# Kernel optimization log

Hardware: AMD Instinct MI355X
Metric: run time of the kernel (lower is better)

Reference implementation:

```python
import jax, jax.numpy as jnp
import numpy as np

L, H, D, V, TMAX = 12, 12, 768, 50257, 1024
B, T = 2, 1024
HD = D // H
EPS = 1e-5


def new_gelu(x):
    return 0.5 * x * (1.0 + jnp.tanh(jnp.sqrt(2.0 / jnp.pi) * (x + 0.044715 * x ** 3)))


def layer_norm(x, w, b):
    mu = jnp.mean(x, axis=-1, keepdims=True)
    var = jnp.var(x, axis=-1, keepdims=True)
    return (x - mu) * jax.lax.rsqrt(var + EPS) * w + b


def setup_inputs() -> dict:
    key = jax.random.key(0)
    ks = jax.random.split(key, 12)
    s = 0.02
    return {
        "idx": jax.random.randint(ks[0], (B, T), 0, V),
        "wte": jax.random.normal(ks[1], (V, D), jnp.float32) * s,
        "wpe": jax.random.normal(ks[2], (TMAX, D), jnp.float32) * s,
        "ln1_w": jnp.ones((L, D), jnp.float32),
        "ln1_b": jnp.zeros((L, D), jnp.float32),
        "attn_w": jax.random.normal(ks[3], (L, D, 3 * D), jnp.float32) * s,
        "attn_b": jnp.zeros((L, 3 * D), jnp.float32),
        "proj_w": jax.random.normal(ks[4], (L, D, D), jnp.float32) * (s / jnp.sqrt(2.0 * L)),
        "proj_b": jnp.zeros((L, D), jnp.float32),
        "ln2_w": jnp.ones((L, D), jnp.float32),
        "ln2_b": jnp.zeros((L, D), jnp.float32),
        "fc_w": jax.random.normal(ks[5], (L, D, 4 * D), jnp.float32) * s,
        "fc_b": jnp.zeros((L, 4 * D), jnp.float32),
        "fc2_w": jax.random.normal(ks[6], (L, 4 * D, D), jnp.float32) * (s / jnp.sqrt(2.0 * L)),
        "fc2_b": jnp.zeros((L, D), jnp.float32),
        "lnf_w": jnp.ones((D,), jnp.float32),
        "lnf_b": jnp.zeros((D,), jnp.float32),
        "lm_head_w": jax.random.normal(ks[7], (D, V), jnp.float32) * s,
    }


def _gpt_forward(idx, wte, wpe, ln1_w, ln1_b, attn_w, attn_b, proj_w, proj_b,
                 ln2_w, ln2_b, fc_w, fc_b, fc2_w, fc2_b, lnf_w, lnf_b, lm_head_w):
    b, t = idx.shape
    x = wte[idx] + wpe[:t][None, :, :]  # [B,T,D]
    causal = jnp.tril(jnp.ones((t, t), bool))  # [T,T]
    scale = 1.0 / jnp.sqrt(jnp.asarray(HD, x.dtype))

    layer_params = {
        "ln1_w": ln1_w, "ln1_b": ln1_b, "attn_w": attn_w, "attn_b": attn_b,
        "proj_w": proj_w, "proj_b": proj_b, "ln2_w": ln2_w, "ln2_b": ln2_b,
        "fc_w": fc_w, "fc_b": fc_b, "fc2_w": fc2_w, "fc2_b": fc2_b,
    }

    def block(x, p):
        h = layer_norm(x, p["ln1_w"], p["ln1_b"])
        qkv = h @ p["attn_w"] + p["attn_b"]  # [B,T,3D]
        q, k, v = jnp.split(qkv, 3, axis=-1)
        q = q.reshape(b, t, H, HD)
        k = k.reshape(b, t, H, HD)
        v = v.reshape(b, t, H, HD)
        att = jnp.einsum("bqhd,bkhd->bhqk", q, k) * scale
        att = jnp.where(causal[None, None, :, :], att, -jnp.inf)
        att = jax.nn.softmax(att, axis=-1)
        y = jnp.einsum("bhqk,bkhd->bqhd", att, v).reshape(b, t, D)
        x = x + y @ p["proj_w"] + p["proj_b"]
        h2 = layer_norm(x, p["ln2_w"], p["ln2_b"])
        m = new_gelu(h2 @ p["fc_w"] + p["fc_b"])
        x = x + m @ p["fc2_w"] + p["fc2_b"]
        return x, None

    x, _ = jax.lax.scan(block, x, layer_params)
    x = layer_norm(x, lnf_w, lnf_b)
    logits = x @ lm_head_w  # [B,T,V]
    return logits


def reference(idx, wte, wpe, ln1_w, ln1_b, attn_w, attn_b, proj_w, proj_b,
              ln2_w, ln2_b, fc_w, fc_b, fc2_w, fc2_b, lnf_w, lnf_b, lm_head_w):
    return _gpt_forward(idx, wte, wpe, ln1_w, ln1_b, attn_w, attn_b, proj_w, proj_b,
                        ln2_w, ln2_b, fc_w, fc_b, fc2_w, fc2_b, lnf_w, lnf_b, lm_head_w)
```

## Files before the change

kernel.cpp:

```cpp
#include <hip/hip_runtime.h>
#include <math.h>

#define Bsz  2
#define Tlen 1024
#define Dm   768
#define Hh   12
#define HDm  64
#define Ll   12
#define Vv   50257
#define Mrows (Bsz * Tlen)

typedef __attribute__((ext_vector_type(8))) short short8;
typedef __attribute__((ext_vector_type(4))) float f32x4;

__device__ __forceinline__ float bf2f(unsigned short u) {
  union { unsigned int i; float f; } v; v.i = ((unsigned int)u) << 16; return v.f;
}
__device__ __forceinline__ unsigned short f2bf(float f) {
  union { float f; unsigned int i; } v; v.f = f;
  unsigned int u = v.i;
  return (unsigned short)((u + 0x7FFFu + ((u >> 16) & 1u)) >> 16);
}
__device__ __forceinline__ float gelu_f(float x) {
  const float c = 0.7978845608028654f;
  return 0.5f * x * (1.0f + tanhf(c * (x + 0.044715f * x * x * x)));
}

__device__ __forceinline__ void gl_lds16(const unsigned short* g, unsigned short* l) {
  __builtin_amdgcn_global_load_lds(
      (const __attribute__((address_space(1))) unsigned int*)g,
      (__attribute__((address_space(3))) unsigned int*)l, 16, 0, 0);
}


__global__ void embed_kernel(const int* __restrict__ idx, const float* __restrict__ wte,
                             const float* __restrict__ wpe, float* __restrict__ x) {
  int i = (blockIdx.x * 256 + threadIdx.x) * 4;
  int d = i % Dm;
  int bt = i / Dm;
  int t = bt % Tlen;
  int tok = idx[bt];
  float4 a = *(const float4*)(wte + (size_t)tok * Dm + d);
  float4 p = *(const float4*)(wpe + (size_t)t * Dm + d);
  float4 r; r.x = a.x + p.x; r.y = a.y + p.y; r.z = a.z + p.z; r.w = a.w + p.w;
  *(float4*)(x + i) = r;
}

__global__ __launch_bounds__(256) void ln_wave(const float* __restrict__ x,
                                               const float* __restrict__ w,
                                               const float* __restrict__ b,
                                               unsigned short* __restrict__ out) {
  int tid = threadIdx.x, wv = tid >> 6, l = tid & 63;
  int row = blockIdx.x * 4 + wv;
  const float* xr = x + (size_t)row * Dm;
  float4 v[3];
  float s = 0.f, s2 = 0.f;
#pragma unroll
  for (int i = 0; i < 3; ++i) {
    v[i] = *(const float4*)(xr + l * 4 + i * 256);
    s += v[i].x + v[i].y + v[i].z + v[i].w;
    s2 += v[i].x * v[i].x + v[i].y * v[i].y + v[i].z * v[i].z + v[i].w * v[i].w;
  }
#pragma unroll
  for (int o = 1; o < 64; o <<= 1) {
    s += __shfl_xor(s, o, 64);
    s2 += __shfl_xor(s2, o, 64);
  }
  float mu = s * (1.0f / Dm);
  float var = s2 * (1.0f / Dm) - mu * mu;
  float rstd = rsqrtf(var + 1e-5f);
  unsigned short* yr = out + (size_t)row * Dm;
#pragma unroll
  for (int i = 0; i < 3; ++i) {
    float4 wv4 = *(const float4*)(w + l * 4 + i * 256);
    float4 bv4 = *(const float4*)(b + l * 4 + i * 256);
    ushort4 o4;
    o4.x = f2bf((v[i].x - mu) * rstd * wv4.x + bv4.x);
    o4.y = f2bf((v[i].y - mu) * rstd * wv4.y + bv4.y);
    o4.z = f2bf((v[i].z - mu) * rstd * wv4.z + bv4.z);
    o4.w = f2bf((v[i].w - mu) * rstd * wv4.w + bv4.w);
    *(ushort4*)(yr + l * 4 + i * 256) = o4;
  }
}

__global__ __launch_bounds__(256) void tconv_kernel(const float* __restrict__ W, int ldw,
                                                    int nValid, unsigned short* __restrict__ WT,
                                                    int K) {
  __shared__ float S[32][33];
  int n0 = blockIdx.x * 32, k0 = blockIdx.y * 32;
  int t = threadIdx.x;
  int nc = t & 31, kr0 = t >> 5;
#pragma unroll
  for (int i = 0; i < 4; ++i) {
    int kr = kr0 + i * 8;
    S[kr][nc] = (n0 + nc < nValid) ? W[(size_t)(k0 + kr) * ldw + n0 + nc] : 0.f;
  }
  __syncthreads();
  int r = t >> 3, c4 = (t & 7) * 4;
  ushort4 o;
  o.x = f2bf(S[c4 + 0][r]); o.y = f2bf(S[c4 + 1][r]);
  o.z = f2bf(S[c4 + 2][r]); o.w = f2bf(S[c4 + 3][r]);
  *(ushort4*)(WT + (size_t)(n0 + r) * K + k0 + c4) = o;
}

__global__ __launch_bounds__(256) void tconv4_kernel(
    const float* __restrict__ wA, const float* __restrict__ wP,
    const float* __restrict__ wF, const float* __restrict__ wF2,
    unsigned short* __restrict__ oA, unsigned short* __restrict__ oP,
    unsigned short* __restrict__ oF, unsigned short* __restrict__ oF2) {
  int bid = blockIdx.x;
  const float* W; unsigned short* WT; int ldw, K, ntn, local;
  if (bid < 1728)      { W = wA;  WT = oA;  ldw = 2304; K = 768;  ntn = 72; local = bid; }
  else if (bid < 2304) { W = wP;  WT = oP;  ldw = 768;  K = 768;  ntn = 24; local = bid - 1728; }
  else if (bid < 4608) { W = wF;  WT = oF;  ldw = 3072; K = 768;  ntn = 96; local = bid - 2304; }
  else                 { W = wF2; WT = oF2; ldw = 768;  K = 3072; ntn = 24; local = bid - 4608; }
  int n0 = (local % ntn) * 32, k0 = (local / ntn) * 32;
  __shared__ float S[32][33];
  int t = threadIdx.x;
  int nc = t & 31, kr0 = t >> 5;
#pragma unroll
  for (int i = 0; i < 4; ++i) {
    int kr = kr0 + i * 8;
    S[kr][nc] = W[(size_t)(k0 + kr) * ldw + n0 + nc];
  }
  __syncthreads();
  int r = t >> 3, c4 = (t & 7) * 4;
  ushort4 o;
  o.x = f2bf(S[c4 + 0][r]); o.y = f2bf(S[c4 + 1][r]);
  o.z = f2bf(S[c4 + 2][r]); o.w = f2bf(S[c4 + 3][r]);
  *(ushort4*)(WT + (size_t)(n0 + r) * K + k0 + c4) = o;
}

template<bool XMAP>
__global__ __launch_bounds__(256) void gemm_big(
    const unsigned short* __restrict__ A, const unsigned short* __restrict__ B, int K,
    const float* __restrict__ bias, const float* __restrict__ res,
    float* __restrict__ outF, unsigned short* __restrict__ outB,
    int ldc, int nValid, int act, int nColTiles) {
  int brow, bcol;
  if (XMAP) {
    int b = blockIdx.x, xcd = b & 7, slot = b >> 3;
    bcol = xcd + 8 * (slot >> 4);
    brow = slot & 15;
    if (bcol >= nColTiles) return;
  } else {
    bcol = blockIdx.x; brow = blockIdx.y;
  }
  __shared__ alignas(16) unsigned short As[2][128][32];
  __shared__ alignas(16) unsigned short Bs[2][128][32];
  int tid = threadIdx.x;
  int rowBase = brow * 128, colBase = bcol * 128;
  int w = tid >> 6, l = tid & 63;
  int wr = w >> 1, wc = w & 1;
  int srow = tid >> 2;
  int skk = (((tid & 3) ^ ((tid >> 3) & 3))) * 8;
  const unsigned short* aSrc = A + (size_t)(rowBase + srow) * K + skk;
  const unsigned short* bSrc = B + (size_t)(colBase + srow) * K + skk;

  f32x4 acc[4][4];
#pragma unroll
  for (int m = 0; m < 4; ++m)
#pragma unroll
    for (int n = 0; n < 4; ++n) acc[m][n] = (f32x4){0.f, 0.f, 0.f, 0.f};

  int fr = l & 15, fq = l >> 4;
  int kslot = (fq ^ ((fr >> 1) & 3)) * 8;

  gl_lds16(aSrc, &As[0][w * 16][0]);
  gl_lds16(aSrc + (size_t)64 * K, &As[0][w * 16 + 64][0]);
  gl_lds16(bSrc, &Bs[0][w * 16][0]);
  gl_lds16(bSrc + (size_t)64 * K, &Bs[0][w * 16 + 64][0]);

  int nIt = K >> 5;
  for (int it = 0; it < nIt; ++it) {
    int cur = it & 1;
    int k0 = it * 32;
    if (it + 1 < nIt) {
      int nx = cur ^ 1;
      gl_lds16(aSrc + k0 + 32, &As[nx][w * 16][0]);
      gl_lds16(aSrc + (size_t)64 * K + k0 + 32, &As[nx][w * 16 + 64][0]);
      gl_lds16(bSrc + k0 + 32, &Bs[nx][w * 16][0]);
      gl_lds16(bSrc + (size_t)64 * K + k0 + 32, &Bs[nx][w * 16 + 64][0]);
      asm volatile("s_waitcnt vmcnt(4)" ::: "memory");
    } else {
      asm volatile("s_waitcnt vmcnt(0)" ::: "memory");
    }
    asm volatile("s_barrier" ::: "memory");

    short8 af[4], bfr[4];
#pragma unroll
    for (int m = 0; m < 4; ++m)
      af[m] = *(const short8*)&As[cur][wr * 64 + m * 16 + fr][kslot];
#pragma unroll
    for (int n = 0; n < 4; ++n)
      bfr[n] = *(const short8*)&Bs[cur][wc * 64 + n * 16 + fr][kslot];
#pragma unroll
    for (int m = 0; m < 4; ++m)
#pragma unroll
      for (int n = 0; n < 4; ++n)
        acc[m][n] = __builtin_amdgcn_mfma_f32_16x16x32_bf16(af[m], bfr[n], acc[m][n], 0, 0, 0);
    asm volatile("s_barrier" ::: "memory");
  }

#pragma unroll
  for (int m = 0; m < 4; ++m) {
    int row = rowBase + wr * 64 + m * 16 + fq * 4;
#pragma unroll
    for (int n = 0; n < 4; ++n) {
      int col = colBase + wc * 64 + n * 16 + fr;
      if (col >= nValid) continue;
      float bv = bias ? bias[col] : 0.f;
#pragma unroll
      for (int j = 0; j < 4; ++j) {
        float v = acc[m][n][j] + bv;
        if (act) v = gelu_f(v);
        if (res) v += res[(size_t)(row + j) * ldc + col];
        if (outF) outF[(size_t)(row + j) * ldc + col] = v;
        else      outB[(size_t)(row + j) * ldc + col] = f2bf(v);
      }
    }
  }
}

__global__ __launch_bounds__(256) void gemm_bf16_sm(
    const unsigned short* __restrict__ A, const unsigned short* __restrict__ B, int K,
    const float* __restrict__ bias,
    float* __restrict__ outF, unsigned short* __restrict__ outB,
    int ldc, int act) {
  __shared__ alignas(16) unsigned short As[2][64][32];
  __shared__ alignas(16) unsigned short Bs[2][128][32];
  int tid = threadIdx.x;
  int rowBase = blockIdx.y * 64;
  int colBase = blockIdx.x * 128;
  int w = tid >> 6, l = tid & 63;
  int fr = l & 15, fq = l >> 4;

  int srow = l >> 2;
  int skk = (((l & 3) ^ ((l >> 3) & 3))) * 8;
  const unsigned short* aSrc = A + (size_t)(rowBase + w * 16 + srow) * K + skk;
  const unsigned short* bSrc = B + (size_t)(colBase + w * 16 + srow) * K + skk;
  int kslot = (fq ^ ((fr >> 1) & 3)) * 8;

  f32x4 acc[4][2];
#pragma unroll
  for (int m = 0; m < 4; ++m)
#pragma unroll
    for (int n = 0; n < 2; ++n) acc[m][n] = (f32x4){0.f, 0.f, 0.f, 0.f};

  gl_lds16(aSrc, &As[0][w * 16][0]);
  gl_lds16(bSrc, &Bs[0][w * 16][0]);
  gl_lds16(bSrc + (size_t)64 * K, &Bs[0][w * 16 + 64][0]);

  int nIt = K >> 5;
  for (int it = 0; it < nIt; ++it) {
    int cur = it & 1;
    int k0 = it * 32;
    if (it + 1 < nIt) {
      int nx = cur ^ 1;
      gl_lds16(aSrc + k0 + 32, &As[nx][w * 16][0]);
      gl_lds16(bSrc + k0 + 32, &Bs[nx][w * 16][0]);
      gl_lds16(bSrc + (size_t)64 * K + k0 + 32, &Bs[nx][w * 16 + 64][0]);
      asm volatile("s_waitcnt vmcnt(3)" ::: "memory");
    } else {
      asm volatile("s_waitcnt vmcnt(0)" ::: "memory");
    }
    asm volatile("s_barrier" ::: "memory");

    short8 af[4], bfr[2];
#pragma unroll
    for (int m = 0; m < 4; ++m)
      af[m] = *(const short8*)&As[cur][m * 16 + fr][kslot];
#pragma unroll
    for (int n = 0; n < 2; ++n)
      bfr[n] = *(const short8*)&Bs[cur][w * 32 + n * 16 + fr][kslot];
#pragma unroll
    for (int m = 0; m < 4; ++m)
#pragma unroll
      for (int n = 0; n < 2; ++n)
        acc[m][n] = __builtin_amdgcn_mfma_f32_16x16x32_bf16(af[m], bfr[n], acc[m][n], 0, 0, 0);
    asm volatile("s_barrier" ::: "memory");
  }

#pragma unroll
  for (int m = 0; m < 4; ++m) {
    int row = rowBase + m * 16 + fq * 4;
#pragma unroll
    for (int n = 0; n < 2; ++n) {
      int col = colBase + w * 32 + n * 16 + fr;
      float bv = bias ? bias[col] : 0.f;
#pragma unroll
      for (int j = 0; j < 4; ++j) {
        float v = acc[m][n][j] + bv;
        if (act) v = gelu_f(v);
        if (outF) outF[(size_t)(row + j) * ldc + col] = v;
        else      outB[(size_t)(row + j) * ldc + col] = f2bf(v);
      }
    }
  }
}

__global__ __launch_bounds__(256) void gemm_splitk(
    const unsigned short* __restrict__ A, const unsigned short* __restrict__ B, int K,
    int Klen, const float* __restrict__ bias, float* __restrict__ outF, int ldc) {
  __shared__ alignas(16) unsigned short As[2][64][32];
  __shared__ alignas(16) unsigned short Bs[2][128][32];
  int tid = threadIdx.x;
  int rowBase = blockIdx.y * 64;
  int colBase = blockIdx.x * 128;
  int Koff = blockIdx.z * Klen;
  int w = tid >> 6, l = tid & 63;
  int fr = l & 15, fq = l >> 4;

  int srow = l >> 2;
  int skk = (((l & 3) ^ ((l >> 3) & 3))) * 8;
  const unsigned short* aSrc = A + (size_t)(rowBase + w * 16 + srow) * K + Koff + skk;
  const unsigned short* bSrc = B + (size_t)(colBase + w * 16 + srow) * K + Koff + skk;
  int kslot = (fq ^ ((fr >> 1) & 3)) * 8;

  f32x4 acc[4][2];
#pragma unroll
  for (int m = 0; m < 4; ++m)
#pragma unroll
    for (int n = 0; n < 2; ++n) acc[m][n] = (f32x4){0.f, 0.f, 0.f, 0.f};

  gl_lds16(aSrc, &As[0][w * 16][0]);
  gl_lds16(bSrc, &Bs[0][w * 16][0]);
  gl_lds16(bSrc + (size_t)64 * K, &Bs[0][w * 16 + 64][0]);

  int nIt = Klen >> 5;
  for (int it = 0; it < nIt; ++it) {
    int cur = it & 1;
    int k0 = it * 32;
    if (it + 1 < nIt) {
      int nx = cur ^ 1;
      gl_lds16(aSrc + k0 + 32, &As[nx][w * 16][0]);
      gl_lds16(bSrc + k0 + 32, &Bs[nx][w * 16][0]);
      gl_lds16(bSrc + (size_t)64 * K + k0 + 32, &Bs[nx][w * 16 + 64][0]);
      asm volatile("s_waitcnt vmcnt(3)" ::: "memory");
    } else {
      asm volatile("s_waitcnt vmcnt(0)" ::: "memory");
    }
    asm volatile("s_barrier" ::: "memory");

    short8 af[4], bfr[2];
#pragma unroll
    for (int m = 0; m < 4; ++m)
      af[m] = *(const short8*)&As[cur][m * 16 + fr][kslot];
#pragma unroll
    for (int n = 0; n < 2; ++n)
      bfr[n] = *(const short8*)&Bs[cur][w * 32 + n * 16 + fr][kslot];
#pragma unroll
    for (int m = 0; m < 4; ++m)
#pragma unroll
      for (int n = 0; n < 2; ++n)
        acc[m][n] = __builtin_amdgcn_mfma_f32_16x16x32_bf16(af[m], bfr[n], acc[m][n], 0, 0, 0);
    asm volatile("s_barrier" ::: "memory");
  }

  bool addBias = (blockIdx.z == 0);
#pragma unroll
  for (int m = 0; m < 4; ++m) {
    int row = rowBase + m * 16 + fq * 4;
#pragma unroll
    for (int n = 0; n < 2; ++n) {
      int col = colBase + w * 32 + n * 16 + fr;
      float bv = addBias ? bias[col] : 0.f;
#pragma unroll
      for (int j = 0; j < 4; ++j) {
        unsafeAtomicAdd(&outF[(size_t)(row + j) * ldc + col], acc[m][n][j] + bv);
      }
    }
  }
}

__global__ __launch_bounds__(256) void attn_mfma(const unsigned short* __restrict__ qkv,
                                                 unsigned short* __restrict__ y) {
  int bx = blockIdx.x;
  int qt = 15 - (bx / 24);
  int bh = bx % 24;
  int h  = bh % Hh;
  int b  = bh / Hh;
  int q0 = qt * 64;
  int tid = threadIdx.x;
  int w = tid >> 6, l = tid & 63;
  int g = l >> 4, fr = l & 15;

  __shared__ alignas(16) unsigned short Kl[2][4096];
  __shared__ alignas(16) unsigned short Vt[4096];
  __shared__ alignas(16) unsigned short Pl[4][1024];

  const size_t rs = 3 * Dm;
  const unsigned short* base = qkv + (size_t)(b * Tlen) * rs + h * HDm;

  short8 qf[2];
  {
    const unsigned short* qrow = base + (size_t)(q0 + w * 16 + fr) * rs;
    qf[0] = *(const short8*)(qrow + g * 8);
    qf[1] = *(const short8*)(qrow + g * 8 + 32);
  }

  int vt_t = tid >> 2, vt_dc = tid & 3;
  uint4 v0r, v1r;

  f32x4 oAcc[4];
#pragma unroll
  for (int nd = 0; nd < 4; ++nd) oAcc[nd] = (f32x4){0.f, 0.f, 0.f, 0.f};
  float mRun[4] = {-1e30f, -1e30f, -1e30f, -1e30f};
  float lRun[4] = {0.f, 0.f, 0.f, 0.f};

  unsigned short* Pw = &Pl[w][0];
  int nkt = qt + 1;

  {
#pragma unroll
    for (int i = 0; i < 2; ++i) {
      int c = i * 256 + tid;
      int t = c >> 3, cl = c & 7;
      int dch = cl ^ (t & 7);
      gl_lds16(base + (size_t)t * rs + Dm + dch * 8, &Kl[0][(i * 256 + w * 64) * 8]);
    }
    const unsigned short* p = base + (size_t)vt_t * rs + 2 * Dm + vt_dc * 16;
    v0r = *(const uint4*)p;
    v1r = *(const uint4*)(p + 8);
  }

  for (int kt = 0; kt < nkt; ++kt) {
    int cur = kt & 1;
    int kbase = kt * 64;
    asm volatile("s_waitcnt vmcnt(0)" ::: "memory");
    __builtin_amdgcn_s_barrier();

    {
      union { uint4 u; unsigned short s[8]; } a, bb;
      a.u = v0r; bb.u = v1r;
#pragma unroll
      for (int j = 0; j < 8; ++j) {
        int d = vt_dc * 16 + j;
        Vt[d * 64 + (vt_t ^ ((d & 7) << 3))] = a.s[j];
        int d2 = d + 8;
        Vt[d2 * 64 + (vt_t ^ ((d2 & 7) << 3))] = bb.s[j];
      }
    }
    if (kt + 1 < nkt) {
      int kb = kbase + 64;
#pragma unroll
      for (int i = 0; i < 2; ++i) {
        int c = i * 256 + tid;
        int t = c >> 3, cl = c & 7;
        int dch = cl ^ (t & 7);
        gl_lds16(base + (size_t)(kb + t) * rs + Dm + dch * 8,
                 &Kl[cur ^ 1][(i * 256 + w * 64) * 8]);
      }
      const unsigned short* p = base + (size_t)(kb + vt_t) * rs + 2 * Dm + vt_dc * 16;
      v0r = *(const uint4*)p;
      v1r = *(const uint4*)(p + 8);
    }
    asm volatile("s_waitcnt lgkmcnt(0)" ::: "memory");
    __builtin_amdgcn_s_barrier();

    f32x4 sAcc[4];
#pragma unroll
    for (int nt = 0; nt < 4; ++nt) sAcc[nt] = (f32x4){0.f, 0.f, 0.f, 0.f};
#pragma unroll
    for (int ks = 0; ks < 2; ++ks)
#pragma unroll
      for (int nt = 0; nt < 4; ++nt) {
        int kcol = nt * 16 + fr;
        short8 kf = *(const short8*)&Kl[cur][kcol * 64 + ((g * 8 + ks * 32) ^ ((kcol & 7) << 3))];
        sAcc[nt] = __builtin_amdgcn_mfma_f32_16x16x32_bf16(qf[ks], kf, sAcc[nt], 0, 0, 0);
      }

    float corr[4];
#pragma unroll
    for (int j = 0; j < 4; ++j) {
      int qg = q0 + w * 16 + g * 4 + j;
      float tm = -1e30f;
#pragma unroll
      for (int nt = 0; nt < 4; ++nt) {
        float s = sAcc[nt][j] * 0.125f;
        int tg = kbase + nt * 16 + fr;
        if (tg > qg) s = -1e30f;
        sAcc[nt][j] = s;
        tm = fmaxf(tm, s);
      }
      tm = fmaxf(tm, __shfl_xor(tm, 1, 16));
      tm = fmaxf(tm, __shfl_xor(tm, 2, 16));
      tm = fmaxf(tm, __shfl_xor(tm, 4, 16));
      tm = fmaxf(tm, __shfl_xor(tm, 8, 16));
      float mN = fmaxf(mRun[j], tm);
      corr[j] = __expf(mRun[j] - mN);
      mRun[j] = mN;
      float ps = 0.f;
#pragma unroll
      for (int nt = 0; nt < 4; ++nt) {
        float p = __expf(sAcc[nt][j] - mN);
        sAcc[nt][j] = p;
        ps += p;
      }
      ps += __shfl_xor(ps, 1, 16);
      ps += __shfl_xor(ps, 2, 16);
      ps += __shfl_xor(ps, 4, 16);
      ps += __shfl_xor(ps, 8, 16);
      lRun[j] = lRun[j] * corr[j] + ps;
    }

#pragma unroll
    for (int nt = 0; nt < 4; ++nt)
#pragma unroll
      for (int j = 0; j < 4; ++j) {
        int q = g * 4 + j;
        int t = nt * 16 + fr;
        Pw[q * 64 + (t ^ ((q & 7) << 3))] = f2bf(sAcc[nt][j]);
      }
#pragma unroll
    for (int nd = 0; nd < 4; ++nd)
#pragma unroll
      for (int j = 0; j < 4; ++j) oAcc[nd][j] *= corr[j];

#pragma unroll
    for (int ks = 0; ks < 2; ++ks) {
      short8 pf = *(const short8*)&Pw[fr * 64 + ((g * 8 + ks * 32) ^ ((fr & 7) << 3))];
#pragma unroll
      for (int nd = 0; nd < 4; ++nd) {
        int d = nd * 16 + fr;
        short8 vf = *(const short8*)&Vt[d * 64 + ((g * 8 + ks * 32) ^ ((fr & 7) << 3))];
        oAcc[nd] = __builtin_amdgcn_mfma_f32_16x16x32_bf16(pf, vf, oAcc[nd], 0, 0, 0);
      }
    }
  }

#pragma unroll
  for (int j = 0; j < 4; ++j) {
    float inv = 1.0f / lRun[j];
    int q = q0 + w * 16 + g * 4 + j;
    unsigned short* yr = y + (size_t)(b * Tlen + q) * Dm + h * HDm + fr;
#pragma unroll
    for (int nd = 0; nd < 4; ++nd)
      yr[nd * 16] = f2bf(oAcc[nd][j] * inv);
  }
}

extern "C" void kernel_launch(void* const* d_in, const int* in_sizes, int n_in,
                              void* d_out, int out_size, void* d_ws, size_t ws_size,
                              hipStream_t stream) {
  const int*   idx    = (const int*)d_in[0];
  const float* wte    = (const float*)d_in[1];
  const float* wpe    = (const float*)d_in[2];
  const float* ln1_w  = (const float*)d_in[3];
  const float* ln1_b  = (const float*)d_in[4];
  const float* attn_w = (const float*)d_in[5];
  const float* attn_b = (const float*)d_in[6];
  const float* proj_w = (const float*)d_in[7];
  const float* proj_b = (const float*)d_in[8];
  const float* ln2_w  = (const float*)d_in[9];
  const float* ln2_b  = (const float*)d_in[10];
  const float* fc_w   = (const float*)d_in[11];
  const float* fc_b   = (const float*)d_in[12];
  const float* fc2_w  = (const float*)d_in[13];
  const float* fc2_b  = (const float*)d_in[14];
  const float* lnf_w  = (const float*)d_in[15];
  const float* lnf_b  = (const float*)d_in[16];
  const float* lmw    = (const float*)d_in[17];
  float* out = (float*)d_out;

  float* x = (float*)d_ws;
  unsigned short* qkvb = (unsigned short*)(x + (size_t)Mrows * Dm);
  unsigned short* xb   = qkvb + (size_t)Mrows * 3 * Dm;
  unsigned short* yb   = xb + (size_t)Mrows * Dm;
  unsigned short* mb   = yb + (size_t)Mrows * Dm;
  unsigned short* wbuf = mb + (size_t)Mrows * 4 * Dm;
  unsigned short* wAttn = wbuf;
  unsigned short* wProj = wAttn + (size_t)3 * Dm * Dm;
  unsigned short* wFc   = wProj + (size_t)Dm * Dm;
  unsigned short* wFc2  = wFc + (size_t)4 * Dm * Dm;

  const size_t baseBytes = (size_t)Mrows * Dm * 4 + (size_t)Mrows * 9 * Dm * 2;
  size_t availShorts = (ws_size - baseBytes) / 2;
  long long cc = (long long)(availShorts / Dm) & ~127LL;
  if (cc > 50304) cc = 50304;
  const int chunkCols = (int)cc;

  embed_kernel<<<(Mrows * Dm) / 1024, 256, 0, stream>>>(idx, wte, wpe, x);

  for (int l = 0; l < Ll; ++l) {
    tconv4_kernel<<<6912, 256, 0, stream>>>(
        attn_w + (size_t)l * Dm * 3 * Dm, proj_w + (size_t)l * Dm * Dm,
        fc_w + (size_t)l * Dm * 4 * Dm, fc2_w + (size_t)l * 4 * Dm * Dm,
        wAttn, wProj, wFc, wFc2);

    ln_wave<<<Mrows / 4, 256, 0, stream>>>(x, ln1_w + l * Dm, ln1_b + l * Dm, xb);
    gemm_bf16_sm<<<dim3(18, 32), 256, 0, stream>>>(xb, wAttn, Dm, attn_b + (size_t)l * 3 * Dm,
                                                   nullptr, qkvb, 3 * Dm, 0);
    attn_mfma<<<Bsz * Hh * 16, 256, 0, stream>>>(qkvb, yb);
    gemm_splitk<<<dim3(6, 32, 2), 256, 0, stream>>>(yb, wProj, Dm, Dm / 2,
                                                    proj_b + (size_t)l * Dm, x, Dm);
    ln_wave<<<Mrows / 4, 256, 0, stream>>>(x, ln2_w + l * Dm, ln2_b + l * Dm, xb);
    gemm_bf16_sm<<<dim3(24, 32), 256, 0, stream>>>(xb, wFc, Dm, fc_b + (size_t)l * 4 * Dm,
                                                   nullptr, mb, 4 * Dm, 1);
    gemm_splitk<<<dim3(6, 32, 2), 256, 0, stream>>>(mb, wFc2, 4 * Dm, 2 * Dm,
                                                    fc2_b + (size_t)l * Dm, x, Dm);
  }

  ln_wave<<<Mrows / 4, 256, 0, stream>>>(x, lnf_w, lnf_b, xb);
  for (int base = 0; base < Vv; base += chunkCols) {
    int ncv = Vv - base; if (ncv > chunkCols) ncv = chunkCols;
    int ntiles = (ncv + 127) / 128;
    tconv_kernel<<<dim3((ncv + 31) / 32, 24), 256, 0, stream>>>(lmw + base, Vv, ncv, wbuf, Dm);
    int cpx = (ntiles + 7) / 8;
    gemm_big<true><<<8 * 16 * cpx, 256, 0, stream>>>(
        xb, wbuf, Dm, nullptr, nullptr, out + base, nullptr, Vv, ncv, 0, ntiles);
  }
}
```

Measured before the change: 2.166 ms.

## Batch all-layer weight conversion into output buffer and widen LM-head GEMM tile

```diff
diff --git a/kernel.cpp b/kernel.cpp
--- a/kernel.cpp
+++ b/kernel.cpp
@@ -9,6 +9,7 @@
 #define Ll   12
 #define Vv   50257
 #define Mrows (Bsz * Tlen)
+#define WPL  7077888
 
 typedef __attribute__((ext_vector_type(8))) short short8;
 typedef __attribute__((ext_vector_type(4))) float f32x4;
@@ -103,17 +104,18 @@
   *(ushort4*)(WT + (size_t)(n0 + r) * K + k0 + c4) = o;
 }
 
-__global__ __launch_bounds__(256) void tconv4_kernel(
-    const float* __restrict__ wA, const float* __restrict__ wP,
-    const float* __restrict__ wF, const float* __restrict__ wF2,
-    unsigned short* __restrict__ oA, unsigned short* __restrict__ oP,
-    unsigned short* __restrict__ oF, unsigned short* __restrict__ oF2) {
+__global__ __launch_bounds__(256) void tconv12_kernel(
+    const float* __restrict__ attn_w, const float* __restrict__ proj_w,
+    const float* __restrict__ fc_w, const float* __restrict__ fc2_w,
+    unsigned short* __restrict__ wAll) {
   int bid = blockIdx.x;
+  int lyr = bid / 6912, rem = bid % 6912;
+  unsigned short* wL = wAll + (size_t)lyr * WPL;
   const float* W; unsigned short* WT; int ldw, K, ntn, local;
-  if (bid < 1728)      { W = wA;  WT = oA;  ldw = 2304; K = 768;  ntn = 72; local = bid; }
-  else if (bid < 2304) { W = wP;  WT = oP;  ldw = 768;  K = 768;  ntn = 24; local = bid - 1728; }
-  else if (bid < 4608) { W = wF;  WT = oF;  ldw = 3072; K = 768;  ntn = 96; local = bid - 2304; }
-  else                 { W = wF2; WT = oF2; ldw = 768;  K = 3072; ntn = 24; local = bid - 4608; }
+  if (rem < 1728)      { W = attn_w + (size_t)lyr * Dm * 3 * Dm; WT = wL;                     ldw = 2304; K = 768;  ntn = 72; local = rem; }
+  else if (rem < 2304) { W = proj_w + (size_t)lyr * Dm * Dm;     WT = wL + 1769472;           ldw = 768;  K = 768;  ntn = 24; local = rem - 1728; }
+  else if (rem < 4608) { W = fc_w + (size_t)lyr * Dm * 4 * Dm;   WT = wL + 1769472 + 589824;  ldw = 3072; K = 768;  ntn = 96; local = rem - 2304; }
+  else                 { W = fc2_w + (size_t)lyr * 4 * Dm * Dm;  WT = wL + 1769472 + 589824 + 2359296; ldw = 768; K = 3072; ntn = 24; local = rem - 4608; }
   int n0 = (local % ntn) * 32, k0 = (local / ntn) * 32;
   __shared__ float S[32][33];
   int t = threadIdx.x;
@@ -132,11 +134,9 @@
 }
 
 template<bool XMAP>
-__global__ __launch_bounds__(256) void gemm_big(
+__global__ __launch_bounds__(256) void gemm_big256(
     const unsigned short* __restrict__ A, const unsigned short* __restrict__ B, int K,
-    const float* __restrict__ bias, const float* __restrict__ res,
-    float* __restrict__ outF, unsigned short* __restrict__ outB,
-    int ldc, int nValid, int act, int nColTiles) {
+    float* __restrict__ outF, int ldc, int nValid, int nColTiles) {
   int brow, bcol;
   if (XMAP) {
     int b = blockIdx.x, xcd = b & 7, slot = b >> 3;
@@ -147,77 +147,72 @@
     bcol = blockIdx.x; brow = blockIdx.y;
   }
   __shared__ alignas(16) unsigned short As[2][128][32];
-  __shared__ alignas(16) unsigned short Bs[2][128][32];
+  __shared__ alignas(16) unsigned short Bs[2][256][32];
   int tid = threadIdx.x;
-  int rowBase = brow * 128, colBase = bcol * 128;
+  int rowBase = brow * 128, colBase = bcol * 256;
   int w = tid >> 6, l = tid & 63;
   int wr = w >> 1, wc = w & 1;
-  int srow = tid >> 2;
-  int skk = (((tid & 3) ^ ((tid >> 3) & 3))) * 8;
-  const unsigned short* aSrc = A + (size_t)(rowBase + srow) * K + skk;
-  const unsigned short* bSrc = B + (size_t)(colBase + srow) * K + skk;
-
-  f32x4 acc[4][4];
+  int srow = l >> 2;
+  int skk = (((l & 3) ^ ((l >> 3) & 3))) * 8;
+  const unsigned short* aSrc = A + (size_t)(rowBase + w * 16 + srow) * K + skk;
+  const unsigned short* bSrc = B + (size_t)(colBase + w * 16 + srow) * K + skk;
+
+  f32x4 acc[4][8];
 #pragma unroll
   for (int m = 0; m < 4; ++m)
 #pragma unroll
-    for (int n = 0; n < 4; ++n) acc[m][n] = (f32x4){0.f, 0.f, 0.f, 0.f};
+    for (int n = 0; n < 8; ++n) acc[m][n] = (f32x4){0.f, 0.f, 0.f, 0.f};
 
   int fr = l & 15, fq = l >> 4;
   int kslot = (fq ^ ((fr >> 1) & 3)) * 8;
 
-  gl_lds16(aSrc, &As[0][w * 16][0]);
-  gl_lds16(aSrc + (size_t)64 * K, &As[0][w * 16 + 64][0]);
-  gl_lds16(bSrc, &Bs[0][w * 16][0]);
-  gl_lds16(bSrc + (size_t)64 * K, &Bs[0][w * 16 + 64][0]);
+#define STG256(k0_, buf_)                                                 \
+  { gl_lds16(aSrc + (k0_), &As[buf_][w * 16][0]);                         \
+    gl_lds16(aSrc + (size_t)64 * K + (k0_), &As[buf_][w * 16 + 64][0]);   \
+    gl_lds16(bSrc + (k0_), &Bs[buf_][w * 16][0]);                         \
+    gl_lds16(bSrc + (size_t)64 * K + (k0_), &Bs[buf_][w * 16 + 64][0]);   \
+    gl_lds16(bSrc + (size_t)128 * K + (k0_), &Bs[buf_][w * 16 + 128][0]); \
+    gl_lds16(bSrc + (size_t)192 * K + (k0_), &Bs[buf_][w * 16 + 192][0]); }
 
   int nIt = K >> 5;
+  STG256(0, 0);
   for (int it = 0; it < nIt; ++it) {
     int cur = it & 1;
     int k0 = it * 32;
     if (it + 1 < nIt) {
-      int nx = cur ^ 1;
-      gl_lds16(aSrc + k0 + 32, &As[nx][w * 16][0]);
-      gl_lds16(aSrc + (size_t)64 * K + k0 + 32, &As[nx][w * 16 + 64][0]);
-      gl_lds16(bSrc + k0 + 32, &Bs[nx][w * 16][0]);
-      gl_lds16(bSrc + (size_t)64 * K + k0 + 32, &Bs[nx][w * 16 + 64][0]);
-      asm volatile("s_waitcnt vmcnt(4)" ::: "memory");
+      STG256(k0 + 32, cur ^ 1);
+      asm volatile("s_waitcnt vmcnt(6)" ::: "memory");
     } else {
       asm volatile("s_waitcnt vmcnt(0)" ::: "memory");
     }
     asm volatile("s_barrier" ::: "memory");
 
-    short8 af[4], bfr[4];
+    short8 af[4], bfr[8];
 #pragma unroll
     for (int m = 0; m < 4; ++m)
       af[m] = *(const short8*)&As[cur][wr * 64 + m * 16 + fr][kslot];
 #pragma unroll
-    for (int n = 0; n < 4; ++n)
-      bfr[n] = *(const short8*)&Bs[cur][wc * 64 + n * 16 + fr][kslot];
+    for (int n = 0; n < 8; ++n)
+      bfr[n] = *(const short8*)&Bs[cur][wc * 128 + n * 16 + fr][kslot];
 #pragma unroll
     for (int m = 0; m < 4; ++m)
 #pragma unroll
-      for (int n = 0; n < 4; ++n)
+      for (int n = 0; n < 8; ++n)
         acc[m][n] = __builtin_amdgcn_mfma_f32_16x16x32_bf16(af[m], bfr[n], acc[m][n], 0, 0, 0);
     asm volatile("s_barrier" ::: "memory");
   }
+#undef STG256
 
 #pragma unroll
   for (int m = 0; m < 4; ++m) {
     int row = rowBase + wr * 64 + m * 16 + fq * 4;
 #pragma unroll
-    for (int n = 0; n < 4; ++n) {
-      int col = colBase + wc * 64 + n * 16 + fr;
+    for (int n = 0; n < 8; ++n) {
+      int col = colBase + wc * 128 + n * 16 + fr;
       if (col >= nValid) continue;
-      float bv = bias ? bias[col] : 0.f;
-#pragma unroll
-      for (int j = 0; j < 4; ++j) {
-        float v = acc[m][n][j] + bv;
-        if (act) v = gelu_f(v);
-        if (res) v += res[(size_t)(row + j) * ldc + col];
-        if (outF) outF[(size_t)(row + j) * ldc + col] = v;
-        else      outB[(size_t)(row + j) * ldc + col] = f2bf(v);
-      }
+#pragma unroll
+      for (int j = 0; j < 4; ++j)
+        outF[(size_t)(row + j) * ldc + col] = acc[m][n][j];
     }
   }
 }
@@ -569,24 +564,25 @@
   unsigned short* yb   = xb + (size_t)Mrows * Dm;
   unsigned short* mb   = yb + (size_t)Mrows * Dm;
   unsigned short* wbuf = mb + (size_t)Mrows * 4 * Dm;
-  unsigned short* wAttn = wbuf;
-  unsigned short* wProj = wAttn + (size_t)3 * Dm * Dm;
-  unsigned short* wFc   = wProj + (size_t)Dm * Dm;
-  unsigned short* wFc2  = wFc + (size_t)4 * Dm * Dm;
+
+  unsigned short* wAll = (unsigned short*)d_out;
 
   const size_t baseBytes = (size_t)Mrows * Dm * 4 + (size_t)Mrows * 9 * Dm * 2;
   size_t availShorts = (ws_size - baseBytes) / 2;
-  long long cc = (long long)(availShorts / Dm) & ~127LL;
-  if (cc > 50304) cc = 50304;
+  long long maxRows = (long long)(availShorts / Dm);
+  long long cc = (maxRows - 256) & ~255LL;
+  if (cc > Vv) cc = Vv;
   const int chunkCols = (int)cc;
 
   embed_kernel<<<(Mrows * Dm) / 1024, 256, 0, stream>>>(idx, wte, wpe, x);
+  tconv12_kernel<<<6912 * Ll, 256, 0, stream>>>(attn_w, proj_w, fc_w, fc2_w, wAll);
 
   for (int l = 0; l < Ll; ++l) {
-    tconv4_kernel<<<6912, 256, 0, stream>>>(
-        attn_w + (size_t)l * Dm * 3 * Dm, proj_w + (size_t)l * Dm * Dm,
-        fc_w + (size_t)l * Dm * 4 * Dm, fc2_w + (size_t)l * 4 * Dm * Dm,
-        wAttn, wProj, wFc, wFc2);
+    unsigned short* wL    = wAll + (size_t)l * WPL;
+    unsigned short* wAttn = wL;
+    unsigned short* wProj = wL + 1769472;
+    unsigned short* wFc   = wL + 1769472 + 589824;
+    unsigned short* wFc2  = wL + 1769472 + 589824 + 2359296;
 
     ln_wave<<<Mrows / 4, 256, 0, stream>>>(x, ln1_w + l * Dm, ln1_b + l * Dm, xb);
     gemm_bf16_sm<<<dim3(18, 32), 256, 0, stream>>>(xb, wAttn, Dm, attn_b + (size_t)l * 3 * Dm,
@@ -604,10 +600,10 @@
   ln_wave<<<Mrows / 4, 256, 0, stream>>>(x, lnf_w, lnf_b, xb);
   for (int base = 0; base < Vv; base += chunkCols) {
     int ncv = Vv - base; if (ncv > chunkCols) ncv = chunkCols;
-    int ntiles = (ncv + 127) / 128;
-    tconv_kernel<<<dim3((ncv + 31) / 32, 24), 256, 0, stream>>>(lmw + base, Vv, ncv, wbuf, Dm);
+    int ntiles = (ncv + 255) / 256;
+    tconv_kernel<<<dim3(ntiles * 8, 24), 256, 0, stream>>>(lmw + base, Vv, ncv, wbuf, Dm);
     int cpx = (ntiles + 7) / 8;
-    gemm_big<true><<<8 * 16 * cpx, 256, 0, stream>>>(
-        xb, wbuf, Dm, nullptr, nullptr, out + base, nullptr, Vv, ncv, 0, ntiles);
-  }
-}
+    gemm_big256<true><<<8 * 16 * cpx, 256, 0, stream>>>(
+        xb, wbuf, Dm, out + base, Vv, ncv, ntiles);
+  }
+}
```

Result: no change. 2.190 ms (+1.1%).
